# Performance work log

Measured on AMD Instinct MI355X. Metric: run time of the kernel, lower is better.

## Reference

```python
import jax, jax.numpy as jnp
import numpy as np

B, N_SITES, N_SYMM, FEATS, LAYERS = 1024, 256, 256, 32, 4


def setup_inputs() -> dict:
    key = jax.random.key(0)
    k1, k2, k3, k4, k5 = jax.random.split(key, 5)
    x_in = jax.random.normal(k1, (B, N_SITES), jnp.float32)
    # Cyclic translation group C_{N_SITES}: perm_g(i) = (i + g) mod N
    i = jnp.arange(N_SITES)
    g = jnp.arange(N_SYMM)
    perms = (i[None, :] + g[:, None]) % N_SITES              # [n_symm, n_sites] int
    # Cayley-table style algebra index: alg[gi, go] = (go - gi) mod n_symm
    group_algebra = ((g[None, :] - g[:, None]) % N_SYMM).reshape(-1)  # [n_symm^2]
    w_symm = jax.random.normal(k2, (N_SITES, FEATS), jnp.float32) / np.sqrt(N_SITES).astype(np.float32)
    b_symm = jax.random.normal(k3, (FEATS,), jnp.float32) * 0.01
    w_eq = jax.random.normal(k4, (LAYERS - 1, N_SYMM, FEATS, FEATS), jnp.float32) / np.sqrt(N_SYMM * FEATS).astype(np.float32)
    b_eq = jax.random.normal(k5, (LAYERS - 1, FEATS), jnp.float32) * 0.01
    return dict(x_in=x_in, perms=perms, group_algebra=group_algebra,
                w_symm=w_symm, b_symm=b_symm, w_eq=w_eq, b_eq=b_eq)


def reference(x_in, perms, group_algebra, w_symm, b_symm, w_eq, b_eq):
    n_symm, n_sites = perms.shape
    feats = w_symm.shape[1]
    # --- DenseSymm: K[g, i, f] = w_symm[perms[g, i], f]  (permutation gather)
    K = jnp.take(w_symm, perms, axis=0)                      # [n_symm, n_sites, feats]
    # y[b, f, g] = sum_i x[b, i] * K[g, i, f] + b_symm[f]
    x = jnp.einsum('bi,gif->bfg', x_in, K) + b_symm[None, :, None]  # [B, feats, n_symm]
    alg = group_algebra.reshape(n_symm, n_symm)              # [gi, go]
    n_layers = w_eq.shape[0]
    for l in range(n_layers):
        # full kernel: Kl[gi, go, fi, fo] = w_eq[l, alg[gi, go], fi, fo]
        Kl = jnp.take(w_eq[l], alg, axis=0)                  # [n_symm, n_symm, feats, feats]
        x = jnp.einsum('bfg,ghfo->boh', x, Kl) + b_eq[l][None, :, None]
        x = jax.nn.swish(x)
    # mean over the flattened (features * n_symm) hidden axis
    return jnp.mean(x, axis=(-2, -1))                        # [B]
```

## Files before the change

### kernel.cpp

```cpp
#include <hip/hip_runtime.h>


#define NG 256
#define FSTR2 258
#define PSLAB (32 * FSTR2 + 2)
#define NLAYER 3

__device__ __forceinline__ int brv6(int x) { return (int)(__brev((unsigned)x) >> 26); }

__device__ __forceinline__ int swz(int a) {
  int h = a >> 4;
  return a ^ ((h ^ (h << 1)) & 15);
}

__device__ __forceinline__ void wave_fft256_lds(float2* __restrict__ s,
                                                const float2* __restrict__ tw,
                                                int lane) {
  asm volatile("s_waitcnt lgkmcnt(0)" ::: "memory");
  #pragma unroll
  for (int t = 0; t < 4; ++t) {
    int i = t * 64 + lane;
    int j = (int)(__brev((unsigned)i) >> 24);
    if (j > i) {
      float2 a = s[swz(i)]; float2 b = s[swz(j)];
      s[swz(i)] = b; s[swz(j)] = a;
    }
  }
  asm volatile("s_waitcnt lgkmcnt(0)" ::: "memory");
  #pragma unroll
  for (int st = 0; st < 8; ++st) {
    const int half = 1 << st;
    const int tshift = 7 - st;
    #pragma unroll
    for (int t = 0; t < 2; ++t) {
      int bf = t * 64 + lane;
      int off = bf & (half - 1);
      int blk = bf >> st;
      int i = (blk << (st + 1)) + off;
      int j = i + half;
      float2 wv = tw[swz(off << tshift)];
      float2 u = s[swz(i)];
      float2 v = s[swz(j)];
      float vr = v.x * wv.x - v.y * wv.y;
      float vi = v.x * wv.y + v.y * wv.x;
      s[swz(i)] = make_float2(u.x + vr, u.y + vi);
      s[swz(j)] = make_float2(u.x - vr, u.y - vi);
    }
    asm volatile("s_waitcnt lgkmcnt(0)" ::: "memory");
  }
}

__global__ __launch_bounds__(256) void gcnn_wfft(
    const float* __restrict__ w_symm, const float* __restrict__ w_eq,
    float2* __restrict__ Ws_hat, float2* __restrict__ WeqM,
    float2* __restrict__ Weq128) {
  __shared__ float2 fbw[4][256];
  __shared__ float2 twl[256];
  const int tid = threadIdx.x;
  const int w = tid >> 6;
  const int lane = tid & 63;
  {
    float a = (float)tid * 0.0245436926f;
    twl[swz(tid)] = make_float2(cosf(a), -sinf(a));
  }
  __syncthreads();
  const int task = blockIdx.x * 4 + w;
  if (task < 32) {
    const int f = task;
    for (int g = lane; g < 256; g += 64)
      fbw[w][swz(g)] = make_float2(w_symm[g * 32 + f], 0.f);
    wave_fft256_lds(&fbw[w][0], twl, lane);
    for (int k = lane; k < 256; k += 64) {
      int pos = brv6(k & 63) | (k & 192);
      Ws_hat[f * 256 + pos] = fbw[w][swz(k)];
    }
  } else {
    const int idx = task - 32;
    const int l = idx >> 10;
    const int fi = (idx >> 5) & 31;
    const int fo = idx & 31;
    for (int g = lane; g < 256; g += 64)
      fbw[w][swz(g)] = make_float2(w_eq[((size_t)(l * 256 + g) * 32 + fi) * 32 + fo] * (1.f / 256.f), 0.f);
    wave_fft256_lds(&fbw[w][0], twl, lane);
    for (int k = lane; k < 129; k += 64) {
      int sk = (k < 64) ? brv6(k) : ((k < 128) ? 64 + brv6(k - 64) : 128);
      if (sk < 128)
        WeqM[((size_t)((l * 32 + fi) * 128 + sk)) * 32 + fo] = fbw[w][swz(k)];
      else
        Weq128[(l * 32 + fi) * 32 + fo] = fbw[w][swz(k)];
    }
  }
}

__device__ __forceinline__ float2 cadd(float2 a, float2 b) { return make_float2(a.x + b.x, a.y + b.y); }
__device__ __forceinline__ float2 csub(float2 a, float2 b) { return make_float2(a.x - b.x, a.y - b.y); }
__device__ __forceinline__ float2 cmul(float2 a, float2 b) {
  return make_float2(a.x * b.x - a.y * b.y, a.x * b.y + a.y * b.x);
}
__device__ __forceinline__ float2 cmulc(float2 a, float2 b) {
  return make_float2(a.x * b.x + a.y * b.y, a.y * b.x - a.x * b.y);
}
__device__ __forceinline__ float2 shxor(float2 v, int m) {
  return make_float2(__shfl_xor(v.x, m), __shfl_xor(v.y, m));
}

__device__ __forceinline__ void fwd256(float2 z[4], const float2 tw[5],
                                       float2 u1, float2 u2, float2 u3, int lane) {
  #pragma unroll
  for (int s = 0; s < 6; ++s) {
    const int half = 32 >> s;
    const bool bot = (lane & half) != 0;
    #pragma unroll
    for (int r = 0; r < 4; ++r) {
      float2 o = shxor(z[r], half);
      float2 sum = cadd(z[r], o);
      float2 dif = csub(o, z[r]);
      float2 bo = (s < 5) ? cmul(dif, tw[s]) : dif;
      z[r] = bot ? bo : sum;
    }
  }
  z[1] = cmul(z[1], u1);
  z[2] = cmul(z[2], u2);
  z[3] = cmul(z[3], u3);
  float2 t0 = cadd(z[0], z[2]), t1 = cadd(z[1], z[3]);
  float2 t2 = csub(z[0], z[2]), t3 = csub(z[1], z[3]);
  z[0] = cadd(t0, t1);
  z[2] = csub(t0, t1);
  z[1] = make_float2(t2.x + t3.y, t2.y - t3.x);
  z[3] = make_float2(t2.x - t3.y, t2.y + t3.x);
}

__device__ __forceinline__ void inv256(float2 z[4], const float2 tw[5],
                                       float2 u1, float2 u2, float2 u3, int lane) {
  float2 t0 = cadd(z[0], z[2]), t1 = cadd(z[1], z[3]);
  float2 t2 = csub(z[0], z[2]), t3 = csub(z[1], z[3]);
  z[0] = cadd(t0, t1);
  z[2] = csub(t0, t1);
  z[1] = make_float2(t2.x - t3.y, t2.y + t3.x);
  z[3] = make_float2(t2.x + t3.y, t2.y - t3.x);
  z[1] = cmulc(z[1], u1);
  z[2] = cmulc(z[2], u2);
  z[3] = cmulc(z[3], u3);
  #pragma unroll
  for (int s = 5; s >= 0; --s) {
    const int half = 32 >> s;
    const bool bot = (lane & half) != 0;
    #pragma unroll
    for (int r = 0; r < 4; ++r) {
      float2 m = (s < 5 && bot) ? cmulc(z[r], tw[s]) : z[r];
      float2 o = shxor(m, half);
      z[r] = bot ? csub(o, m) : cadd(o, m);
    }
  }
}

__device__ __forceinline__ float swishf(float y) { return y / (1.f + __expf(-y)); }

__global__ __launch_bounds__(512, 1) void gcnn_main(
    const float* __restrict__ x_in, const float* __restrict__ b_symm,
    const float* __restrict__ b_eq, const float2* __restrict__ Ws_hat,
    const float2* __restrict__ WeqM, const float2* __restrict__ Weq128,
    float* __restrict__ out) {
  __shared__ float2 Zs[2 * PSLAB];
  __shared__ float2 fxz[2 * 260];
  __shared__ float red[8][4];

  const int tid = threadIdx.x;
  const int w = tid >> 6;
  const int lane = tid & 63;
  const int brev = brv6(lane);

  float2 tw[5];
  #pragma unroll
  for (int s = 0; s < 5; ++s) {
    const int half = 32 >> s;
    float ang = -0.09817477042468103871f * (float)((lane & (half - 1)) << s);
    __sincosf(ang, &tw[s].y, &tw[s].x);
  }
  float2 u1;
  {
    float ang = -0.02454369260617025968f * (float)brev;
    __sincosf(ang, &u1.y, &u1.x);
  }
  const float2 u2 = cmul(u1, u1);
  const float2 u3 = cmul(u2, u1);
  const int rbl = brv6((64 - brev) & 63);

  if (w < 2) {
    const float* xa = x_in + (size_t)(blockIdx.x * 4 + 2 * w) * NG;
    float4 va = reinterpret_cast<const float4*>(xa)[lane];
    float4 vb = reinterpret_cast<const float4*>(xa + NG)[lane];
    float2 z[4] = {{va.x, vb.x}, {va.y, vb.y}, {va.z, vb.z}, {va.w, vb.w}};
    fwd256(z, tw, u1, u2, u3, lane);
    fxz[w * 260 + lane] = z[0];
    fxz[w * 260 + 64 + lane] = z[1];
    fxz[w * 260 + 128 + lane] = z[2];
    fxz[w * 260 + 192 + lane] = z[3];
  }
  __syncthreads();

  for (int t = w; t < 64; t += 8) {
    const int p = t >> 5;
    const int f = t & 31;
    const float bs = 256.f * b_symm[f];
    float2* zrow = Zs + p * PSLAB + f * FSTR2;
    const float2* wsf = Ws_hat + f * 256;
    const float2* fx = fxz + p * 260;
    #pragma unroll
    for (int r = 0; r < 4; ++r) {
      const int s = lane + (r << 6);
      const int m = (lane == 0) ? (((4 - r) & 3) << 6) : (rbl + ((3 - r) << 6));
      float2 o = cmul(fx[m], wsf[s]);
      if (s == 0) { o.x += bs; o.y += bs; }
      zrow[s] = o;
    }
    if (lane < 2) zrow[256 + lane] = make_float2(0.f, 0.f);
  }
  __syncthreads();

  #pragma unroll 1
  for (int l = 0; l < NLAYER; ++l) {
    const bool last = (l == NLAYER - 1);

    {
      const int kp = tid >> 2;
      const int p  = (tid >> 1) & 1;
      const int hf = tid & 1;
      const int lq = kp & 63;
      int spart;
      if (lq == 0) spart = (kp == 0) ? 256 : 192;
      else spart = brv6((64 - brv6(lq)) & 63) + ((3 - (kp >> 6)) << 6);
      float2 alo[16], ahi[16];
      #pragma unroll
      for (int j = 0; j < 16; ++j) {
        alo[j] = make_float2(0.f, 0.f);
        ahi[j] = make_float2(0.f, 0.f);
      }
      const float2* zb = Zs + p * PSLAB;
      #pragma unroll 2
      for (int fi = 0; fi < 32; ++fi) {
        float2 h0 = zb[fi * FSTR2 + kp];
        float2 h1 = zb[fi * FSTR2 + spart];
        const float4* wp = reinterpret_cast<const float4*>(
            WeqM + ((size_t)((l * 32 + fi) * 128 + kp)) * 32 + hf * 16);
        #pragma unroll
        for (int q = 0; q < 8; ++q) {
          float4 v = wp[q];
          alo[2 * q].x     += h0.x * v.x - h0.y * v.y;
          alo[2 * q].y     += h0.x * v.y + h0.y * v.x;
          ahi[2 * q].x     += h1.x * v.x + h1.y * v.y;
          ahi[2 * q].y     += h1.y * v.x - h1.x * v.y;
          alo[2 * q + 1].x += h0.x * v.z - h0.y * v.w;
          alo[2 * q + 1].y += h0.x * v.w + h0.y * v.z;
          ahi[2 * q + 1].x += h1.x * v.z + h1.y * v.w;
          ahi[2 * q + 1].y += h1.y * v.z - h1.x * v.w;
        }
      }
      if (kp == 0) {
        #pragma unroll
        for (int j = 0; j < 16; ++j) {
          float be = b_eq[l * 32 + hf * 16 + j];
          alo[j].x += be;
          alo[j].y += be;
        }
      }
      float2* zw = Zs + p * PSLAB;
      #pragma unroll
      for (int j = 0; j < 16; ++j) {
        zw[(hf * 16 + j) * FSTR2 + kp] = alo[j];
        zw[(hf * 16 + j) * FSTR2 + spart] = ahi[j];
      }
      if (w == 0) {
        const int pp = lane >> 5;
        const int fo = lane & 31;
        float2 a = make_float2(0.f, 0.f);
        #pragma unroll 4
        for (int fi = 0; fi < 32; ++fi) {
          float2 h = Zs[pp * PSLAB + fi * FSTR2 + 128];
          float2 v = Weq128[(l * 32 + fi) * 32 + fo];
          a.x += h.x * v.x - h.y * v.y;
          a.y += h.x * v.y + h.y * v.x;
        }
        Zs[pp * PSLAB + fo * FSTR2 + 128] = a;
      }
    }
    __syncthreads();

    float ls00 = 0.f, ls01 = 0.f, ls10 = 0.f, ls11 = 0.f;
    for (int t = w; t < 64; t += 8) {
      const int p = t >> 5;
      const int f = t & 31;
      float2* zrow = Zs + p * PSLAB + f * FSTR2;
      float2 z[4];
      #pragma unroll
      for (int r = 0; r < 4; ++r) z[r] = zrow[lane + (r << 6)];
      inv256(z, tw, u1, u2, u3, lane);
      if (!last) {
        #pragma unroll
        for (int r = 0; r < 4; ++r) {
          z[r].x = swishf(z[r].x);
          z[r].y = swishf(z[r].y);
        }
        fwd256(z, tw, u1, u2, u3, lane);
        #pragma unroll
        for (int r = 0; r < 4; ++r) zrow[lane + (r << 6)] = z[r];
      } else {
        float sa = 0.f, sb = 0.f;
        #pragma unroll
        for (int r = 0; r < 4; ++r) {
          sa += swishf(z[r].x);
          sb += swishf(z[r].y);
        }
        if (t < 32) { ls00 += sa; ls01 += sb; }
        else        { ls10 += sa; ls11 += sb; }
      }
    }
    if (last) {
      #pragma unroll
      for (int m = 32; m >= 1; m >>= 1) {
        ls00 += __shfl_xor(ls00, m);
        ls01 += __shfl_xor(ls01, m);
        ls10 += __shfl_xor(ls10, m);
        ls11 += __shfl_xor(ls11, m);
      }
      if (lane == 0) {
        red[w][0] = ls00; red[w][1] = ls01;
        red[w][2] = ls10; red[w][3] = ls11;
      }
    }
    __syncthreads();
  }

  if (tid < 4) {
    float s = 0.f;
    #pragma unroll
    for (int ww = 0; ww < 8; ++ww) s += red[ww][tid];
    out[blockIdx.x * 4 + tid] = s * (1.f / 8192.f);
  }
}

extern "C" void kernel_launch(void* const* d_in, const int* in_sizes, int n_in,
                              void* d_out, int out_size, void* d_ws, size_t ws_size,
                              hipStream_t stream) {
  const float* x_in   = (const float*)d_in[0];
  const float* w_symm = (const float*)d_in[3];
  const float* b_symm = (const float*)d_in[4];
  const float* w_eq   = (const float*)d_in[5];
  const float* b_eq   = (const float*)d_in[6];
  float* out = (float*)d_out;

  float2* Ws_hat = (float2*)d_ws;
  float2* WeqM   = Ws_hat + 32 * 256;
  float2* Weq128 = WeqM + (size_t)3 * 32 * 128 * 32;

  hipLaunchKernelGGL(gcnn_wfft, dim3(776), dim3(256), 0, stream,
                     w_symm, w_eq, Ws_hat, WeqM, Weq128);
  hipLaunchKernelGGL(gcnn_main, dim3(256), dim3(512), 0, stream,
                     x_in, b_symm, b_eq, Ws_hat, WeqM, Weq128, out);
}
```

Measured before the change: 177.7 us.

## Halve batch per block, split input-feature reduction across lanes, shrink LDS

Result: slower. 267.5 us (+50.5%).

```diff
diff --git a/kernel.cpp b/kernel.cpp
--- a/kernel.cpp
+++ b/kernel.cpp
@@ -2,8 +2,6 @@
 
 
 #define NG 256
-#define FSTR2 258
-#define PSLAB (32 * FSTR2 + 2)
 #define NLAYER 3
 
 __device__ __forceinline__ int brv6(int x) { return (int)(__brev((unsigned)x) >> 26); }
@@ -156,14 +154,12 @@
 
 __device__ __forceinline__ float swishf(float y) { return y / (1.f + __expf(-y)); }
 
-__global__ __launch_bounds__(512, 1) void gcnn_main(
+__global__ __launch_bounds__(512, 4) void gcnn_main(
     const float* __restrict__ x_in, const float* __restrict__ b_symm,
     const float* __restrict__ b_eq, const float2* __restrict__ Ws_hat,
     const float2* __restrict__ WeqM, const float2* __restrict__ Weq128,
     float* __restrict__ out) {
-  __shared__ float2 Zs[2 * PSLAB];
-  __shared__ float2 fxz[2 * 260];
-  __shared__ float red[8][4];
+  __shared__ float2 Zs[32 * 256];
 
   const int tid = threadIdx.x;
   const int w = tid >> 6;
@@ -186,37 +182,60 @@
   const float2 u3 = cmul(u2, u1);
   const int rbl = brv6((64 - brev) & 63);
 
-  if (w < 2) {
-    const float* xa = x_in + (size_t)(blockIdx.x * 4 + 2 * w) * NG;
+  if (w == 0) {
+    const float* xa = x_in + (size_t)blockIdx.x * 2 * NG;
     float4 va = reinterpret_cast<const float4*>(xa)[lane];
     float4 vb = reinterpret_cast<const float4*>(xa + NG)[lane];
     float2 z[4] = {{va.x, vb.x}, {va.y, vb.y}, {va.z, vb.z}, {va.w, vb.w}};
     fwd256(z, tw, u1, u2, u3, lane);
-    fxz[w * 260 + lane] = z[0];
-    fxz[w * 260 + 64 + lane] = z[1];
-    fxz[w * 260 + 128 + lane] = z[2];
-    fxz[w * 260 + 192 + lane] = z[3];
+    float2 mz[4];
+    #pragma unroll
+    for (int r = 0; r < 4; ++r) {
+      float2 g = make_float2(__shfl(z[3 - r].x, rbl), __shfl(z[3 - r].y, rbl));
+      mz[r] = g;
+    }
+    if (lane == 0) {
+      float2 own[4] = {z[0], z[1], z[2], z[3]};
+      #pragma unroll
+      for (int r = 0; r < 4; ++r) mz[r] = own[(4 - r) & 3];
+    }
+    #pragma unroll
+    for (int r = 0; r < 4; ++r) Zs[31 * 256 + lane + (r << 6)] = mz[r];
   }
   __syncthreads();
 
-  for (int t = w; t < 64; t += 8) {
-    const int p = t >> 5;
-    const int f = t & 31;
-    const float bs = 256.f * b_symm[f];
-    float2* zrow = Zs + p * PSLAB + f * FSTR2;
-    const float2* wsf = Ws_hat + f * 256;
-    const float2* fx = fxz + p * 260;
-    #pragma unroll
-    for (int r = 0; r < 4; ++r) {
-      const int s = lane + (r << 6);
-      const int m = (lane == 0) ? (((4 - r) & 3) << 6) : (rbl + ((3 - r) << 6));
-      float2 o = cmul(fx[m], wsf[s]);
-      if (s == 0) { o.x += bs; o.y += bs; }
-      zrow[s] = o;
-    }
-    if (lane < 2) zrow[256 + lane] = make_float2(0.f, 0.f);
+  {
+    float2 keep[4];
+    #pragma unroll
+    for (int j = 0; j < 4; ++j) {
+      const int f = w + 8 * j;
+      const float bs = 256.f * b_symm[f];
+      const float2* wsf = Ws_hat + f * 256;
+      float2 o[4];
+      #pragma unroll
+      for (int r = 0; r < 4; ++r) {
+        const int s = lane + (r << 6);
+        float2 m = Zs[31 * 256 + s];
+        o[r] = cmul(m, wsf[s]);
+        if (s == 0) { o[r].x += bs; o[r].y += bs; }
+      }
+      if (f == 31) {
+        #pragma unroll
+        for (int r = 0; r < 4; ++r) keep[r] = o[r];
+      } else {
+        #pragma unroll
+        for (int r = 0; r < 4; ++r) Zs[f * 256 + lane + (r << 6)] = o[r];
+      }
+    }
+    __syncthreads();
+    if (w == 7) {
+      #pragma unroll
+      for (int r = 0; r < 4; ++r) Zs[31 * 256 + lane + (r << 6)] = keep[r];
+    }
   }
   __syncthreads();
+
+  float outv0 = 0.f, outv1 = 0.f;
 
   #pragma unroll 1
   for (int l = 0; l < NLAYER; ++l) {
@@ -224,11 +243,11 @@
 
     {
       const int kp = tid >> 2;
-      const int p  = (tid >> 1) & 1;
+      const int fh = (tid >> 1) & 1;
       const int hf = tid & 1;
       const int lq = kp & 63;
       int spart;
-      if (lq == 0) spart = (kp == 0) ? 256 : 192;
+      if (lq == 0) spart = (kp == 0) ? 0 : 192;
       else spart = brv6((64 - brv6(lq)) & 63) + ((3 - (kp >> 6)) << 6);
       float2 alo[16], ahi[16];
       #pragma unroll
@@ -236,11 +255,11 @@
         alo[j] = make_float2(0.f, 0.f);
         ahi[j] = make_float2(0.f, 0.f);
       }
-      const float2* zb = Zs + p * PSLAB;
       #pragma unroll 2
-      for (int fi = 0; fi < 32; ++fi) {
-        float2 h0 = zb[fi * FSTR2 + kp];
-        float2 h1 = zb[fi * FSTR2 + spart];
+      for (int f2 = 0; f2 < 16; ++f2) {
+        const int fi = fh * 16 + f2;
+        float2 h0 = Zs[fi * 256 + kp];
+        float2 h1 = Zs[fi * 256 + spart];
         const float4* wp = reinterpret_cast<const float4*>(
             WeqM + ((size_t)((l * 32 + fi) * 128 + kp)) * 32 + hf * 16);
         #pragma unroll
@@ -256,41 +275,46 @@
           ahi[2 * q + 1].y += h1.y * v.z - h1.x * v.w;
         }
       }
-      if (kp == 0) {
+      #pragma unroll
+      for (int j = 0; j < 16; ++j) {
+        alo[j] = cadd(alo[j], shxor(alo[j], 2));
+        ahi[j] = cadd(ahi[j], shxor(ahi[j], 2));
+      }
+      if (fh == 0) {
+        if (kp == 0) {
+          #pragma unroll
+          for (int j = 0; j < 16; ++j) {
+            float be = b_eq[l * 32 + hf * 16 + j];
+            alo[j].x += be;
+            alo[j].y += be;
+          }
+        }
         #pragma unroll
         for (int j = 0; j < 16; ++j) {
-          float be = b_eq[l * 32 + hf * 16 + j];
-          alo[j].x += be;
-          alo[j].y += be;
-        }
-      }
-      float2* zw = Zs + p * PSLAB;
-      #pragma unroll
-      for (int j = 0; j < 16; ++j) {
-        zw[(hf * 16 + j) * FSTR2 + kp] = alo[j];
-        zw[(hf * 16 + j) * FSTR2 + spart] = ahi[j];
-      }
-      if (w == 0) {
-        const int pp = lane >> 5;
-        const int fo = lane & 31;
+          Zs[(hf * 16 + j) * 256 + kp] = alo[j];
+          if (kp != 0) Zs[(hf * 16 + j) * 256 + spart] = ahi[j];
+        }
+      }
+      if (w == 0 && lane < 32) {
+        const int fo = lane;
         float2 a = make_float2(0.f, 0.f);
         #pragma unroll 4
         for (int fi = 0; fi < 32; ++fi) {
-          float2 h = Zs[pp * PSLAB + fi * FSTR2 + 128];
+          float2 h = Zs[fi * 256 + 128];
           float2 v = Weq128[(l * 32 + fi) * 32 + fo];
           a.x += h.x * v.x - h.y * v.y;
           a.y += h.x * v.y + h.y * v.x;
         }
-        Zs[pp * PSLAB + fo * FSTR2 + 128] = a;
+        Zs[fo * 256 + 128] = a;
       }
     }
     __syncthreads();
 
-    float ls00 = 0.f, ls01 = 0.f, ls10 = 0.f, ls11 = 0.f;
-    for (int t = w; t < 64; t += 8) {
-      const int p = t >> 5;
-      const int f = t & 31;
-      float2* zrow = Zs + p * PSLAB + f * FSTR2;
+    float ls0 = 0.f, ls1 = 0.f;
+    #pragma unroll 1
+    for (int j = 0; j < 4; ++j) {
+      const int f = w + 8 * j;
+      float2* zrow = Zs + f * 256;
       float2 z[4];
       #pragma unroll
       for (int r = 0; r < 4; ++r) z[r] = zrow[lane + (r << 6)];
@@ -305,37 +329,31 @@
         #pragma unroll
         for (int r = 0; r < 4; ++r) zrow[lane + (r << 6)] = z[r];
       } else {
-        float sa = 0.f, sb = 0.f;
         #pragma unroll
         for (int r = 0; r < 4; ++r) {
-          sa += swishf(z[r].x);
-          sb += swishf(z[r].y);
-        }
-        if (t < 32) { ls00 += sa; ls01 += sb; }
-        else        { ls10 += sa; ls11 += sb; }
+          ls0 += swishf(z[r].x);
+          ls1 += swishf(z[r].y);
+        }
       }
     }
     if (last) {
       #pragma unroll
       for (int m = 32; m >= 1; m >>= 1) {
-        ls00 += __shfl_xor(ls00, m);
-        ls01 += __shfl_xor(ls01, m);
-        ls10 += __shfl_xor(ls10, m);
-        ls11 += __shfl_xor(ls11, m);
-      }
-      if (lane == 0) {
-        red[w][0] = ls00; red[w][1] = ls01;
-        red[w][2] = ls10; red[w][3] = ls11;
-      }
+        ls0 += __shfl_xor(ls0, m);
+        ls1 += __shfl_xor(ls1, m);
+      }
+      __syncthreads();
+      if (lane == 0) Zs[w] = make_float2(ls0, ls1);
     }
     __syncthreads();
   }
 
-  if (tid < 4) {
+  if (tid < 2) {
     float s = 0.f;
     #pragma unroll
-    for (int ww = 0; ww < 8; ++ww) s += red[ww][tid];
-    out[blockIdx.x * 4 + tid] = s * (1.f / 8192.f);
+    for (int ww = 0; ww < 8; ++ww)
+      s += (tid == 0) ? Zs[ww].x : Zs[ww].y;
+    out[blockIdx.x * 2 + tid] = s * (1.f / 8192.f);
   }
 }
 
@@ -355,6 +373,6 @@
 
   hipLaunchKernelGGL(gcnn_wfft, dim3(776), dim3(256), 0, stream,
                      w_symm, w_eq, Ws_hat, WeqM, Weq128);
-  hipLaunchKernelGGL(gcnn_main, dim3(256), dim3(512), 0, stream,
+  hipLaunchKernelGGL(gcnn_main, dim3(512), dim3(512), 0, stream,
                      x_in, b_symm, b_eq, Ws_hat, WeqM, Weq128, out);
 }
```

## Remap frequency-domain channel mixing so each thread owns one frequency position

Applied to the files above, without the earlier changes.

Measured after the change: 457.6 us. +157.5%, slower.

```diff
diff --git a/kernel.cpp b/kernel.cpp
--- a/kernel.cpp
+++ b/kernel.cpp
@@ -223,65 +223,68 @@
     const bool last = (l == NLAYER - 1);
 
     {
-      const int kp = tid >> 2;
-      const int p  = (tid >> 1) & 1;
+      const int pos = tid >> 1;
       const int hf = tid & 1;
-      const int lq = kp & 63;
-      int spart;
-      if (lq == 0) spart = (kp == 0) ? 256 : 192;
-      else spart = brv6((64 - brv6(lq)) & 63) + ((3 - (kp >> 6)) << 6);
-      float2 alo[16], ahi[16];
-      #pragma unroll
-      for (int j = 0; j < 16; ++j) {
-        alo[j] = make_float2(0.f, 0.f);
-        ahi[j] = make_float2(0.f, 0.f);
-      }
-      const float2* zb = Zs + p * PSLAB;
-      #pragma unroll 2
-      for (int fi = 0; fi < 32; ++fi) {
-        float2 h0 = zb[fi * FSTR2 + kp];
-        float2 h1 = zb[fi * FSTR2 + spart];
-        const float4* wp = reinterpret_cast<const float4*>(
-            WeqM + ((size_t)((l * 32 + fi) * 128 + kp)) * 32 + hf * 16);
-        #pragma unroll
-        for (int q = 0; q < 8; ++q) {
-          float4 v = wp[q];
-          alo[2 * q].x     += h0.x * v.x - h0.y * v.y;
-          alo[2 * q].y     += h0.x * v.y + h0.y * v.x;
-          ahi[2 * q].x     += h1.x * v.x + h1.y * v.y;
-          ahi[2 * q].y     += h1.y * v.x - h1.x * v.y;
-          alo[2 * q + 1].x += h0.x * v.z - h0.y * v.w;
-          alo[2 * q + 1].y += h0.x * v.w + h0.y * v.z;
-          ahi[2 * q + 1].x += h1.x * v.z + h1.y * v.w;
-          ahi[2 * q + 1].y += h1.y * v.z - h1.x * v.w;
+      const int lq = pos & 63;
+      const int q6 = brv6(lq);
+      const int b = q6 | (pos & 192);
+      int wpos;
+      float sg;
+      if (b < 128)      { wpos = pos; sg = 1.f; }
+      else if (b == 128){ wpos = -1;  sg = 1.f; }
+      else {
+        wpos = (lq == 0) ? 64 : (brv6((64 - q6) & 63) + ((3 - (pos >> 6)) << 6));
+        sg = -1.f;
+      }
+      #pragma unroll 1
+      for (int p = 0; p < 2; ++p) {
+        float2* zslab = Zs + p * PSLAB;
+        float2 acc[16];
+        #pragma unroll
+        for (int j = 0; j < 16; ++j) acc[j] = make_float2(0.f, 0.f);
+        if (wpos < 0) {
+          const float2* wb = Weq128 + l * 1024 + hf * 16;
+          #pragma unroll 2
+          for (int fi = 0; fi < 32; ++fi) {
+            float2 h = zslab[fi * FSTR2 + 128];
+            const float4* wp = reinterpret_cast<const float4*>(wb + fi * 32);
+            #pragma unroll
+            for (int q = 0; q < 8; ++q) {
+              float4 v = wp[q];
+              acc[2 * q].x     += h.x * v.x - h.y * v.y;
+              acc[2 * q].y     += h.x * v.y + h.y * v.x;
+              acc[2 * q + 1].x += h.x * v.z - h.y * v.w;
+              acc[2 * q + 1].y += h.x * v.w + h.y * v.z;
+            }
+          }
+        } else {
+          #pragma unroll 2
+          for (int fi = 0; fi < 32; ++fi) {
+            float2 h = zslab[fi * FSTR2 + pos];
+            const float hxs = sg * h.x, hys = sg * h.y;
+            const float4* wp = reinterpret_cast<const float4*>(
+                WeqM + ((size_t)((l * 32 + fi) * 128 + wpos)) * 32 + hf * 16);
+            #pragma unroll
+            for (int q = 0; q < 8; ++q) {
+              float4 v = wp[q];
+              acc[2 * q].x     += h.x * v.x - hys * v.y;
+              acc[2 * q].y     += hxs * v.y + h.y * v.x;
+              acc[2 * q + 1].x += h.x * v.z - hys * v.w;
+              acc[2 * q + 1].y += hxs * v.w + h.y * v.z;
+            }
+          }
+          if (pos == 0) {
+            #pragma unroll
+            for (int j = 0; j < 16; ++j) {
+              float be = b_eq[l * 32 + hf * 16 + j];
+              acc[j].x += be;
+              acc[j].y += be;
+            }
+          }
         }
-      }
-      if (kp == 0) {
-        #pragma unroll
-        for (int j = 0; j < 16; ++j) {
-          float be = b_eq[l * 32 + hf * 16 + j];
-          alo[j].x += be;
-          alo[j].y += be;
-        }
-      }
-      float2* zw = Zs + p * PSLAB;
-      #pragma unroll
-      for (int j = 0; j < 16; ++j) {
-        zw[(hf * 16 + j) * FSTR2 + kp] = alo[j];
-        zw[(hf * 16 + j) * FSTR2 + spart] = ahi[j];
-      }
-      if (w == 0) {
-        const int pp = lane >> 5;
-        const int fo = lane & 31;
-        float2 a = make_float2(0.f, 0.f);
-        #pragma unroll 4
-        for (int fi = 0; fi < 32; ++fi) {
-          float2 h = Zs[pp * PSLAB + fi * FSTR2 + 128];
-          float2 v = Weq128[(l * 32 + fi) * 32 + fo];
-          a.x += h.x * v.x - h.y * v.y;
-          a.y += h.x * v.y + h.y * v.x;
-        }
-        Zs[pp * PSLAB + fo * FSTR2 + 128] = a;
+        #pragma unroll
+        for (int j = 0; j < 16; ++j)
+          zslab[(hf * 16 + j) * FSTR2 + pos] = acc[j];
       }
     }
     __syncthreads();
```
